# Kernel optimization log

Measured on AMD Instinct MI355X. Metric: run time of the kernel, lower is better.

Reference implementation:

```python
import jax, jax.numpy as jnp
import numpy as np

RFF_DIM = 256
ATTENTION_SCALE = 0.1
LAMBDA_REG = 0.01
SIGMA = 1.0


def setup_inputs() -> dict:
    key = jax.random.key(0)
    k1, k2, k3 = jax.random.split(key, 3)
    N, D_IN = 262144, 64
    Z = jax.random.normal(k1, (N, D_IN), dtype=jnp.float32)
    W_rff = jax.random.normal(k2, (D_IN, RFF_DIM), dtype=jnp.float32)
    A = jax.random.normal(k3, (2 * RFF_DIM, 3), dtype=jnp.float32) * 0.01
    return {"Z": Z, "W_rff": W_rff, "A": A}


def reference(Z, W_rff, A):
    # --- RFF transform: Q = sqrt(1/R) * [cos(Z W / sigma), sin(Z W / sigma)] ---
    proj = (Z @ W_rff) / SIGMA                       # [N, R]
    Q = jnp.sqrt(1.0 / RFF_DIM) * jnp.concatenate(
        [jnp.cos(proj), jnp.sin(proj)], axis=-1)      # [N, 2R]

    N, F = Q.shape
    chunk = max(F // RFF_DIM, 1)                      # = 2 here
    n_chunks = F // chunk                             # = RFF_DIM

    # --- convexified attention over feature chunks (vectorized) ---
    Qc = Q.reshape(N, n_chunks, chunk)                # [N, K, c]
    A_mean = jnp.mean(A, axis=-1)                     # [2R]
    # per-chunk trace score: mean over batch of <Q_i, A_mean[:c]>
    scores = jnp.mean(jnp.einsum('nkc,c->nk', Qc, A_mean[:chunk]), axis=0)  # [K]
    alpha = jax.nn.softmax(scores / (ATTENTION_SCALE * np.sqrt(RFF_DIM)))   # [K]
    # per-chunk reweighting (dim-preserving recombination)
    Q_tilde = (alpha[None, :, None] * Qc).reshape(N, F)                      # [N, 2R]

    # --- small GEMM head + nuclear-norm regularizer ---
    predictions = Q_tilde @ A                          # [N, out]
    AW = jax.nn.softmax(predictions / np.sqrt(RFF_DIM), axis=-1)
    nuclear_norm = jnp.sum(jnp.linalg.svd(A, compute_uv=False))
    reg_loss = LAMBDA_REG * nuclear_norm
    return predictions, AW, reg_loss, alpha
```

## Files before the change

### kernel.cpp

```cpp
#include <hip/hip_runtime.h>
#include <math.h>

#define N_ROWS 262144
#define D_IN 64
#define RFF 256
#define NTILES (N_ROWS / 16)
#define GRID_BIG 768
#define NWAVES (GRID_BIG * 4)

#define OFF_PRED 0
#define OFF_AW (N_ROWS * 3)
#define OFF_REG (2 * N_ROWS * 3)
#define OFF_ALPHA (2 * N_ROWS * 3 + 1)

#define WS_B 512
#define WS_WF 1280

typedef _Float16 f16x8 __attribute__((ext_vector_type(8)));
typedef float f32x4 __attribute__((ext_vector_type(4)));
typedef float f32x2 __attribute__((ext_vector_type(2)));

__device__ __forceinline__ f32x4 mfma16(f16x8 a, f16x8 b, f32x4 c) {
    return __builtin_amdgcn_mfma_f32_16x16x32_f16(a, b, c, 0, 0, 0);
}

__device__ __forceinline__ unsigned short f32_to_bf16_rne(float x) {
    unsigned int u = __float_as_uint(x);
    unsigned int r = u + 0x7fffu + ((u >> 16) & 1u);
    return (unsigned short)(r >> 16);
}

__device__ __forceinline__ void sincos_rev(float pr, float& sn, float& cs) {
    float f;
    asm("v_fract_f32 %0, %1" : "=v"(f) : "v"(pr));
    asm("v_sin_f32 %0, %1" : "=v"(sn) : "v"(f));
    asm("v_cos_f32 %0, %1" : "=v"(cs) : "v"(f));
}

__device__ __forceinline__ void gload_lds16(const float* g, float* lds) {
    __builtin_amdgcn_global_load_lds(
        (const __attribute__((address_space(1))) unsigned int*)g,
        (__attribute__((address_space(3))) unsigned int*)(lds), 16, 0, 0);
}

#define WAITVM0() do { asm volatile("s_waitcnt vmcnt(0)" ::: "memory"); \
                       __builtin_amdgcn_sched_barrier(0); } while (0)
#define LGKM0()   do { asm volatile("s_waitcnt lgkmcnt(0)" ::: "memory"); \
                       __builtin_amdgcn_sched_barrier(0); } while (0)

__global__ __launch_bounds__(256) void k_prep(const float* __restrict__ W,
                                              float* __restrict__ ws) {
    const int e = blockIdx.x * 256 + threadIdx.x;
    if (e < 512) ws[e] = 0.f;
    const int lane = e & 63;
    const int slot = e >> 6;
    const int kh = slot & 1;
    const int ct = slot >> 1;
    const int k0 = kh * 32 + 8 * (lane >> 4);
    const int col = ct * 16 + (lane & 15);
    f16x8 v;
#pragma unroll
    for (int i = 0; i < 8; ++i)
        v[i] = (_Float16)(W[(k0 + i) * RFF + col] * 0.15915494309189535f);
    *(f16x8*)(ws + WS_WF + e * 4) = v;
}

__device__ __forceinline__ void dma_Bf(const float* __restrict__ wsWf, float* Bff,
                                       int wv, int l) {
#pragma unroll
    for (int m = 0; m < 8; ++m) {
        const int off = wv * 2048 + m * 256;
        gload_lds16(wsWf + off + l * 4, Bff + off);
    }
}

__device__ __forceinline__ void stage_dma(const float* __restrict__ Z, int n0, int l,
                                          float* ldsbase) {
#pragma unroll
    for (int m = 0; m < 4; ++m) {
        const int row = m * 4 + (l >> 4);
        const int gc = (l & 15) ^ (row & 7);
        gload_lds16(Z + (size_t)(n0 + row) * D_IN + gc * 4, ldsbase + m * 256);
    }
}

__device__ __forceinline__ void frags_from_lds(const float* bb, int lr, int lh,
                                               f16x8& ah0, f16x8& ah1) {
    const int s4 = lr & 7;
    const float* rp = bb + lr * 64;
    float z[16];
    *(float4*)&z[0]  = *(const float4*)(rp + (((lh * 2 + 0) ^ s4) << 2));
    *(float4*)&z[4]  = *(const float4*)(rp + (((lh * 2 + 1) ^ s4) << 2));
    *(float4*)&z[8]  = *(const float4*)(rp + (((lh * 2 + 8) ^ s4) << 2));
    *(float4*)&z[12] = *(const float4*)(rp + (((lh * 2 + 9) ^ s4) << 2));
    LGKM0();
#pragma unroll
    for (int i = 0; i < 8; ++i) {
        ah0[i] = (_Float16)z[i];
        ah1[i] = (_Float16)z[8 + i];
    }
}

__global__ __launch_bounds__(256, 3) void k_pass1(const float* __restrict__ Z,
                                                  const float* __restrict__ ws_in,
                                                  float* __restrict__ U) {
    __shared__ float Bff[8192];
    __shared__ float Zs[4][1024];
    __shared__ float Ured[512];
    const int t = threadIdx.x;
    const int wv = t >> 6, l = t & 63, lr = l & 15, lh = l >> 4;

    dma_Bf(ws_in + WS_WF, Bff, wv, l);
    const int gwid = blockIdx.x * 4 + wv;
    const int tstart = gwid * 5 + (gwid < 1024 ? gwid : 1024);
    const int tcnt = 5 + (gwid < 1024 ? 1 : 0);
    stage_dma(Z, tstart * 16, l, &Zs[wv][0]);
    Ured[t] = 0.f;
    Ured[t + 256] = 0.f;
    __syncthreads();

    const f16x8* Bf = (const f16x8*)Bff;
    f32x2 accC2[16], accS2[16];
#pragma unroll
    for (int c = 0; c < 16; ++c) { accC2[c] = (f32x2){0.f, 0.f}; accS2[c] = (f32x2){0.f, 0.f}; }

    for (int tt = 0; tt < tcnt; ++tt) {
        if (tt) WAITVM0();
        f16x8 ah0, ah1;
        frags_from_lds(&Zs[wv][0], lr, lh, ah0, ah1);
        if (tt + 1 < tcnt) {
            stage_dma(Z, (tstart + tt + 1) * 16, l, &Zs[wv][0]);
            __builtin_amdgcn_sched_barrier(0);
        }
        f32x4 acc[16];
#pragma unroll
        for (int ct = 0; ct < 16; ++ct) acc[ct] = (f32x4){0.f, 0.f, 0.f, 0.f};
#pragma unroll
        for (int ct = 0; ct < 16; ++ct) {
            acc[ct] = mfma16(ah0, Bf[(ct * 2 + 0) * 64 + l], acc[ct]);
            acc[ct] = mfma16(ah1, Bf[(ct * 2 + 1) * 64 + l], acc[ct]);
        }
#pragma unroll
        for (int ct = 0; ct < 16; ++ct) {
            float sn0, cs0, sn1, cs1, sn2, cs2, sn3, cs3;
            sincos_rev(acc[ct][0], sn0, cs0);
            sincos_rev(acc[ct][1], sn1, cs1);
            sincos_rev(acc[ct][2], sn2, cs2);
            sincos_rev(acc[ct][3], sn3, cs3);
            accC2[ct] += (f32x2){cs0, cs1};
            accC2[ct] += (f32x2){cs2, cs3};
            accS2[ct] += (f32x2){sn0, sn1};
            accS2[ct] += (f32x2){sn2, sn3};
        }
    }
#pragma unroll
    for (int ct = 0; ct < 16; ++ct) {
        float c = accC2[ct][0] + accC2[ct][1];
        float s = accS2[ct][0] + accS2[ct][1];
        c += __shfl_xor(c, 16);
        c += __shfl_xor(c, 32);
        s += __shfl_xor(s, 16);
        s += __shfl_xor(s, 32);
        if (l < 16) {
            atomicAdd(&Ured[ct * 16 + l], c * 0.0625f);
            atomicAdd(&Ured[256 + ct * 16 + l], s * 0.0625f);
        }
    }
    __syncthreads();
    atomicAdd(&U[t], Ured[t]);
    atomicAdd(&U[t + 256], Ured[t + 256]);
}

__global__ __launch_bounds__(256) void k_alpha(const float* __restrict__ U,
                                               const float* __restrict__ A,
                                               float* __restrict__ ws,
                                               float* __restrict__ out) {
    __shared__ float sm[256];
    __shared__ double gred[256];
    __shared__ double G6[6];
    const int k = threadIdx.x;

    const float am0 = (A[0] + A[1] + A[2]) * (1.0f / 3.0f);
    const float am1 = (A[3] + A[4] + A[5]) * (1.0f / 3.0f);
    float score = (am0 * U[2 * k] + am1 * U[2 * k + 1]) * (1.0f / (float)N_ROWS);
    float x = score * (1.0f / 1.6f);

    sm[k] = x;
    __syncthreads();
    for (int s = 128; s > 0; s >>= 1) {
        if (k < s) sm[k] = fmaxf(sm[k], sm[k + s]);
        __syncthreads();
    }
    float mx = sm[0];
    __syncthreads();
    float e = __expf(x - mx);
    sm[k] = e;
    __syncthreads();
    for (int s = 128; s > 0; s >>= 1) {
        if (k < s) sm[k] += sm[k + s];
        __syncthreads();
    }
    float al = e / sm[0];
    out[OFF_ALPHA + k] = al;
    sm[k] = al;
    __syncthreads();

    {
        const float ac = 0.0625f * sm[k >> 1];
        const float as = 0.0625f * sm[128 + (k >> 1)];
        unsigned int* BtP = (unsigned int*)(ws + WS_B);
#pragma unroll
        for (int j = 0; j < 3; ++j) {
            float bc = ac * A[k * 3 + j];
            float bs = as * A[(256 + k) * 3 + j];
            unsigned int ulo = f32_to_bf16_rne(bc);
            unsigned int uhi = f32_to_bf16_rne(bs);
            BtP[k * 3 + j] = ulo | (uhi << 16);
        }
    }

    double af[2][3];
#pragma unroll
    for (int t2 = 0; t2 < 2; ++t2)
#pragma unroll
        for (int j = 0; j < 3; ++j) af[t2][j] = (double)A[(k + t2 * 256) * 3 + j];
    const int ei[6] = {0, 0, 0, 1, 1, 2};
    const int ej[6] = {0, 1, 2, 1, 2, 2};
    for (int eidx = 0; eidx < 6; ++eidx) {
        double p = af[0][ei[eidx]] * af[0][ej[eidx]] + af[1][ei[eidx]] * af[1][ej[eidx]];
        gred[k] = p;
        __syncthreads();
        for (int s = 128; s > 0; s >>= 1) {
            if (k < s) gred[k] += gred[k + s];
            __syncthreads();
        }
        if (k == 0) G6[eidx] = gred[0];
        __syncthreads();
    }
    if (k == 0) {
        double g00 = G6[0], g01 = G6[1], g02 = G6[2], g11 = G6[3], g12 = G6[4], g22 = G6[5];
        double q = (g00 + g11 + g22) / 3.0;
        double p1 = g01 * g01 + g02 * g02 + g12 * g12;
        double p2 = (g00 - q) * (g00 - q) + (g11 - q) * (g11 - q) + (g22 - q) * (g22 - q) + 2.0 * p1;
        double nuc;
        if (p2 < 1e-300) {
            nuc = 3.0 * sqrt(fmax(q, 0.0));
        } else {
            double p = sqrt(p2 / 6.0);
            double b00 = (g00 - q) / p, b11 = (g11 - q) / p, b22 = (g22 - q) / p;
            double b01 = g01 / p, b02 = g02 / p, b12 = g12 / p;
            double detB = b00 * (b11 * b22 - b12 * b12) - b01 * (b01 * b22 - b12 * b02) +
                          b02 * (b01 * b12 - b11 * b02);
            double rr = detB / 2.0;
            rr = fmin(1.0, fmax(-1.0, rr));
            double phi = acos(rr) / 3.0;
            double e1 = q + 2.0 * p * cos(phi);
            double e3 = q + 2.0 * p * cos(phi + 2.0943951023931953);
            double e2 = 3.0 * q - e1 - e3;
            nuc = sqrt(fmax(e1, 0.0)) + sqrt(fmax(e2, 0.0)) + sqrt(fmax(e3, 0.0));
        }
        out[OFF_REG] = (float)(0.01 * nuc);
    }
}

__global__ __launch_bounds__(256, 3) void k_pass2(const float* __restrict__ Z,
                                                  const float* __restrict__ ws_in,
                                                  float* __restrict__ out) {
    __shared__ float Bff[8192];
    __shared__ float Zs[4][1024];
    __shared__ unsigned int BtP[768];
    const int t = threadIdx.x;
    const int wv = t >> 6, l = t & 63, lr = l & 15, lh = l >> 4;

    dma_Bf(ws_in + WS_WF, Bff, wv, l);
    const int gwid = blockIdx.x * 4 + wv;
    const int tstart = gwid * 5 + (gwid < 1024 ? gwid : 1024);
    const int tcnt = 5 + (gwid < 1024 ? 1 : 0);
    stage_dma(Z, tstart * 16, l, &Zs[wv][0]);
    {
        const unsigned int* src = (const unsigned int*)(ws_in + WS_B);
        BtP[t] = src[t];
        BtP[t + 256] = src[t + 256];
        BtP[t + 512] = src[t + 512];
    }
    __syncthreads();

    const f16x8* Bf = (const f16x8*)Bff;

    for (int tt = 0; tt < tcnt; ++tt) {
        const int n0 = (tstart + tt) * 16;
        if (tt) WAITVM0();
        f16x8 ah0, ah1;
        frags_from_lds(&Zs[wv][0], lr, lh, ah0, ah1);
        if (tt + 1 < tcnt) {
            stage_dma(Z, (tstart + tt + 1) * 16, l, &Zs[wv][0]);
            __builtin_amdgcn_sched_barrier(0);
        }
        f32x4 acc[16];
#pragma unroll
        for (int ct = 0; ct < 16; ++ct) acc[ct] = (f32x4){0.f, 0.f, 0.f, 0.f};
#pragma unroll
        for (int ct = 0; ct < 16; ++ct) {
            acc[ct] = mfma16(ah0, Bf[(ct * 2 + 0) * 64 + l], acc[ct]);
            acc[ct] = mfma16(ah1, Bf[(ct * 2 + 1) * 64 + l], acc[ct]);
        }
        f32x2 pa01[3], pa23[3];
#pragma unroll
        for (int j = 0; j < 3; ++j) { pa01[j] = (f32x2){0.f, 0.f}; pa23[j] = (f32x2){0.f, 0.f}; }
#pragma unroll
        for (int ct = 0; ct < 16; ++ct) {
            const int f = ct * 16 + lr;
            unsigned int u0 = BtP[f * 3 + 0], u1 = BtP[f * 3 + 1], u2 = BtP[f * 3 + 2];
            float sn0, cs0, sn1, cs1, sn2, cs2, sn3, cs3;
            sincos_rev(acc[ct][0], sn0, cs0);
            sincos_rev(acc[ct][1], sn1, cs1);
            sincos_rev(acc[ct][2], sn2, cs2);
            sincos_rev(acc[ct][3], sn3, cs3);
            const f32x2 cs01 = {cs0, cs1}, cs23 = {cs2, cs3};
            const f32x2 sn01 = {sn0, sn1}, sn23 = {sn2, sn3};
            const float bcf[3] = {__uint_as_float(u0 << 16), __uint_as_float(u1 << 16),
                                  __uint_as_float(u2 << 16)};
            const float bsf[3] = {__uint_as_float(u0 & 0xffff0000u),
                                  __uint_as_float(u1 & 0xffff0000u),
                                  __uint_as_float(u2 & 0xffff0000u)};
#pragma unroll
            for (int j = 0; j < 3; ++j) {
                const f32x2 bc2 = {bcf[j], bcf[j]};
                const f32x2 bs2 = {bsf[j], bsf[j]};
                pa01[j] = __builtin_elementwise_fma(
                    cs01, bc2, __builtin_elementwise_fma(sn01, bs2, pa01[j]));
                pa23[j] = __builtin_elementwise_fma(
                    cs23, bc2, __builtin_elementwise_fma(sn23, bs2, pa23[j]));
            }
        }
        float pa[4][3];
#pragma unroll
        for (int j = 0; j < 3; ++j) {
            pa[0][j] = pa01[j][0];
            pa[1][j] = pa01[j][1];
            pa[2][j] = pa23[j][0];
            pa[3][j] = pa23[j][1];
        }
#pragma unroll
        for (int r = 0; r < 4; ++r)
#pragma unroll
            for (int j = 0; j < 3; ++j) {
                pa[r][j] += __shfl_xor(pa[r][j], 1);
                pa[r][j] += __shfl_xor(pa[r][j], 2);
                pa[r][j] += __shfl_xor(pa[r][j], 4);
                pa[r][j] += __shfl_xor(pa[r][j], 8);
            }
        float q0 = 0.f, q1 = 0.f, q2 = 0.f;
#pragma unroll
        for (int r = 0; r < 4; ++r)
            if (lr == r) { q0 = pa[r][0]; q1 = pa[r][1]; q2 = pa[r][2]; }
        if (lr < 4) {
            const size_t n = (size_t)n0 + 4 * lh + lr;
            out[OFF_PRED + n * 3 + 0] = q0;
            out[OFF_PRED + n * 3 + 1] = q1;
            out[OFF_PRED + n * 3 + 2] = q2;
            float x0 = q0 * 0.0625f, x1 = q1 * 0.0625f, x2 = q2 * 0.0625f;
            float m = fmaxf(x0, fmaxf(x1, x2));
            float e0 = __expf(x0 - m), e1 = __expf(x1 - m), e2 = __expf(x2 - m);
            float inv = 1.0f / (e0 + e1 + e2);
            out[OFF_AW + n * 3 + 0] = e0 * inv;
            out[OFF_AW + n * 3 + 1] = e1 * inv;
            out[OFF_AW + n * 3 + 2] = e2 * inv;
        }
    }
}

extern "C" void kernel_launch(void* const* d_in, const int* in_sizes, int n_in,
                              void* d_out, int out_size, void* d_ws, size_t ws_size,
                              hipStream_t stream) {
    const float* Z = (const float*)d_in[0];
    const float* W = (const float*)d_in[1];
    const float* A = (const float*)d_in[2];
    float* out = (float*)d_out;
    float* ws = (float*)d_ws;

    hipLaunchKernelGGL(k_prep, dim3(8), dim3(256), 0, stream, W, ws);
    hipLaunchKernelGGL(k_pass1, dim3(GRID_BIG), dim3(256), 0, stream, Z, ws, ws);
    hipLaunchKernelGGL(k_alpha, dim3(1), dim3(256), 0, stream, ws, A, ws, out);
    hipLaunchKernelGGL(k_pass2, dim3(GRID_BIG), dim3(256), 0, stream, Z, ws, out);
}
```

Baseline: 88.82 us.

## Split RFF features across block pairs, fold alpha into pass2, add softmax kernel

```diff
diff --git a/kernel.cpp b/kernel.cpp
--- a/kernel.cpp
+++ b/kernel.cpp
@@ -5,15 +5,13 @@
 #define D_IN 64
 #define RFF 256
 #define NTILES (N_ROWS / 16)
-#define GRID_BIG 768
-#define NWAVES (GRID_BIG * 4)
+#define GRID 1024
 
 #define OFF_PRED 0
 #define OFF_AW (N_ROWS * 3)
 #define OFF_REG (2 * N_ROWS * 3)
 #define OFF_ALPHA (2 * N_ROWS * 3 + 1)
 
-#define WS_B 512
 #define WS_WF 1280
 
 typedef _Float16 f16x8 __attribute__((ext_vector_type(8)));
@@ -65,12 +63,12 @@
     *(f16x8*)(ws + WS_WF + e * 4) = v;
 }
 
-__device__ __forceinline__ void dma_Bf(const float* __restrict__ wsWf, float* Bff,
-                                       int wv, int l) {
-#pragma unroll
-    for (int m = 0; m < 8; ++m) {
-        const int off = wv * 2048 + m * 256;
-        gload_lds16(wsWf + off + l * 4, Bff + off);
+__device__ __forceinline__ void dma_Bf_half(const float* __restrict__ wsWf, float* Bf,
+                                            int h, int wv, int l) {
+#pragma unroll
+    for (int m = 0; m < 4; ++m) {
+        const int off = wv * 1024 + m * 256;
+        gload_lds16(wsWf + h * 4096 + off + l * 4, Bf + off);
     }
 }
 
@@ -101,221 +99,212 @@
     }
 }
 
-__global__ __launch_bounds__(256, 3) void k_pass1(const float* __restrict__ Z,
+__global__ __launch_bounds__(256, 4) void k_pass1(const float* __restrict__ Z,
                                                   const float* __restrict__ ws_in,
                                                   float* __restrict__ U) {
-    __shared__ float Bff[8192];
+    __shared__ float Bff[4096];
     __shared__ float Zs[4][1024];
-    __shared__ float Ured[512];
+    __shared__ float Ured[256];
     const int t = threadIdx.x;
     const int wv = t >> 6, l = t & 63, lr = l & 15, lh = l >> 4;
-
-    dma_Bf(ws_in + WS_WF, Bff, wv, l);
-    const int gwid = blockIdx.x * 4 + wv;
-    const int tstart = gwid * 5 + (gwid < 1024 ? gwid : 1024);
-    const int tcnt = 5 + (gwid < 1024 ? 1 : 0);
+    const int h = blockIdx.x & 1;
+    const int g = blockIdx.x >> 1;
+
+    dma_Bf_half(ws_in + WS_WF, Bff, h, wv, l);
+    const int tstart = g * 32 + wv * 8;
     stage_dma(Z, tstart * 16, l, &Zs[wv][0]);
     Ured[t] = 0.f;
-    Ured[t + 256] = 0.f;
     __syncthreads();
 
     const f16x8* Bf = (const f16x8*)Bff;
-    f32x2 accC2[16], accS2[16];
-#pragma unroll
-    for (int c = 0; c < 16; ++c) { accC2[c] = (f32x2){0.f, 0.f}; accS2[c] = (f32x2){0.f, 0.f}; }
-
-    for (int tt = 0; tt < tcnt; ++tt) {
+    f32x2 accC2[8], accS2[8];
+#pragma unroll
+    for (int c = 0; c < 8; ++c) { accC2[c] = (f32x2){0.f, 0.f}; accS2[c] = (f32x2){0.f, 0.f}; }
+
+    for (int tt = 0; tt < 8; ++tt) {
         if (tt) WAITVM0();
         f16x8 ah0, ah1;
         frags_from_lds(&Zs[wv][0], lr, lh, ah0, ah1);
-        if (tt + 1 < tcnt) {
+        if (tt + 1 < 8) {
             stage_dma(Z, (tstart + tt + 1) * 16, l, &Zs[wv][0]);
             __builtin_amdgcn_sched_barrier(0);
         }
-        f32x4 acc[16];
-#pragma unroll
-        for (int ct = 0; ct < 16; ++ct) acc[ct] = (f32x4){0.f, 0.f, 0.f, 0.f};
-#pragma unroll
-        for (int ct = 0; ct < 16; ++ct) {
-            acc[ct] = mfma16(ah0, Bf[(ct * 2 + 0) * 64 + l], acc[ct]);
-            acc[ct] = mfma16(ah1, Bf[(ct * 2 + 1) * 64 + l], acc[ct]);
-        }
-#pragma unroll
-        for (int ct = 0; ct < 16; ++ct) {
+        f32x4 acc[8];
+#pragma unroll
+        for (int c = 0; c < 8; ++c) acc[c] = (f32x4){0.f, 0.f, 0.f, 0.f};
+#pragma unroll
+        for (int c = 0; c < 8; ++c) {
+            acc[c] = mfma16(ah0, Bf[(c * 2 + 0) * 64 + l], acc[c]);
+            acc[c] = mfma16(ah1, Bf[(c * 2 + 1) * 64 + l], acc[c]);
+        }
+#pragma unroll
+        for (int c = 0; c < 8; ++c) {
             float sn0, cs0, sn1, cs1, sn2, cs2, sn3, cs3;
-            sincos_rev(acc[ct][0], sn0, cs0);
-            sincos_rev(acc[ct][1], sn1, cs1);
-            sincos_rev(acc[ct][2], sn2, cs2);
-            sincos_rev(acc[ct][3], sn3, cs3);
-            accC2[ct] += (f32x2){cs0, cs1};
-            accC2[ct] += (f32x2){cs2, cs3};
-            accS2[ct] += (f32x2){sn0, sn1};
-            accS2[ct] += (f32x2){sn2, sn3};
-        }
-    }
-#pragma unroll
-    for (int ct = 0; ct < 16; ++ct) {
-        float c = accC2[ct][0] + accC2[ct][1];
-        float s = accS2[ct][0] + accS2[ct][1];
-        c += __shfl_xor(c, 16);
-        c += __shfl_xor(c, 32);
-        s += __shfl_xor(s, 16);
-        s += __shfl_xor(s, 32);
+            sincos_rev(acc[c][0], sn0, cs0);
+            sincos_rev(acc[c][1], sn1, cs1);
+            sincos_rev(acc[c][2], sn2, cs2);
+            sincos_rev(acc[c][3], sn3, cs3);
+            accC2[c] += (f32x2){cs0, cs1};
+            accC2[c] += (f32x2){cs2, cs3};
+            accS2[c] += (f32x2){sn0, sn1};
+            accS2[c] += (f32x2){sn2, sn3};
+        }
+    }
+#pragma unroll
+    for (int c = 0; c < 8; ++c) {
+        float cc = accC2[c][0] + accC2[c][1];
+        float ss = accS2[c][0] + accS2[c][1];
+        cc += __shfl_xor(cc, 16);
+        cc += __shfl_xor(cc, 32);
+        ss += __shfl_xor(ss, 16);
+        ss += __shfl_xor(ss, 32);
         if (l < 16) {
-            atomicAdd(&Ured[ct * 16 + l], c * 0.0625f);
-            atomicAdd(&Ured[256 + ct * 16 + l], s * 0.0625f);
-        }
-    }
-    __syncthreads();
-    atomicAdd(&U[t], Ured[t]);
-    atomicAdd(&U[t + 256], Ured[t + 256]);
-}
-
-__global__ __launch_bounds__(256) void k_alpha(const float* __restrict__ U,
-                                               const float* __restrict__ A,
-                                               float* __restrict__ ws,
-                                               float* __restrict__ out) {
-    __shared__ float sm[256];
-    __shared__ double gred[256];
+            atomicAdd(&Ured[c * 16 + l], cc * 0.0625f);
+            atomicAdd(&Ured[128 + c * 16 + l], ss * 0.0625f);
+        }
+    }
+    __syncthreads();
+    if (t < 128) atomicAdd(&U[128 * h + t], Ured[t]);
+    else atomicAdd(&U[256 + 128 * h + (t - 128)], Ured[t]);
+}
+
+__global__ __launch_bounds__(256, 4) void k_pass2(const float* __restrict__ Z,
+                                                  const float* __restrict__ ws_in,
+                                                  const float* __restrict__ A,
+                                                  float* __restrict__ out) {
+    __shared__ float Bff[4096];
+    __shared__ float Zs[4][1024];
+    __shared__ float sca[256];
+    __shared__ unsigned int BtP[384];
     __shared__ double G6[6];
-    const int k = threadIdx.x;
+    const int t = threadIdx.x;
+    const int wv = t >> 6, l = t & 63, lr = l & 15, lh = l >> 4;
+    const int h = blockIdx.x & 1;
+    const int g = blockIdx.x >> 1;
+
+    dma_Bf_half(ws_in + WS_WF, Bff, h, wv, l);
 
     const float am0 = (A[0] + A[1] + A[2]) * (1.0f / 3.0f);
     const float am1 = (A[3] + A[4] + A[5]) * (1.0f / 3.0f);
-    float score = (am0 * U[2 * k] + am1 * U[2 * k + 1]) * (1.0f / (float)N_ROWS);
-    float x = score * (1.0f / 1.6f);
-
-    sm[k] = x;
+    float x = (am0 * ws_in[2 * t] + am1 * ws_in[2 * t + 1]) *
+              (1.0f / (float)N_ROWS) * (1.0f / 1.6f);
+    sca[t] = x;
     __syncthreads();
     for (int s = 128; s > 0; s >>= 1) {
-        if (k < s) sm[k] = fmaxf(sm[k], sm[k + s]);
+        if (t < s) sca[t] = fmaxf(sca[t], sca[t + s]);
         __syncthreads();
     }
-    float mx = sm[0];
+    float mx = sca[0];
     __syncthreads();
     float e = __expf(x - mx);
-    sm[k] = e;
+    sca[t] = e;
     __syncthreads();
     for (int s = 128; s > 0; s >>= 1) {
-        if (k < s) sm[k] += sm[k + s];
+        if (t < s) sca[t] += sca[t + s];
         __syncthreads();
     }
-    float al = e / sm[0];
-    out[OFF_ALPHA + k] = al;
-    sm[k] = al;
-    __syncthreads();
-
-    {
-        const float ac = 0.0625f * sm[k >> 1];
-        const float as = 0.0625f * sm[128 + (k >> 1)];
-        unsigned int* BtP = (unsigned int*)(ws + WS_B);
+    float al = e / sca[0];
+    __syncthreads();
+    sca[t] = al;
+    __syncthreads();
+
+    if (blockIdx.x == 0) {
+        out[OFF_ALPHA + t] = al;
+        double* gred = (double*)&Zs[0][0];
+        double af[2][3];
+#pragma unroll
+        for (int t2 = 0; t2 < 2; ++t2)
+#pragma unroll
+            for (int j = 0; j < 3; ++j) af[t2][j] = (double)A[(t + t2 * 256) * 3 + j];
+        const int ei[6] = {0, 0, 0, 1, 1, 2};
+        const int ej[6] = {0, 1, 2, 1, 2, 2};
+        for (int eidx = 0; eidx < 6; ++eidx) {
+            double p = af[0][ei[eidx]] * af[0][ej[eidx]] + af[1][ei[eidx]] * af[1][ej[eidx]];
+            gred[t] = p;
+            __syncthreads();
+            for (int s = 128; s > 0; s >>= 1) {
+                if (t < s) gred[t] += gred[t + s];
+                __syncthreads();
+            }
+            if (t == 0) G6[eidx] = gred[0];
+            __syncthreads();
+        }
+        if (t == 0) {
+            double g00 = G6[0], g01 = G6[1], g02 = G6[2], g11 = G6[3], g12 = G6[4], g22 = G6[5];
+            double q = (g00 + g11 + g22) / 3.0;
+            double p1 = g01 * g01 + g02 * g02 + g12 * g12;
+            double p2 = (g00 - q) * (g00 - q) + (g11 - q) * (g11 - q) +
+                        (g22 - q) * (g22 - q) + 2.0 * p1;
+            double nuc;
+            if (p2 < 1e-300) {
+                nuc = 3.0 * sqrt(fmax(q, 0.0));
+            } else {
+                double p = sqrt(p2 / 6.0);
+                double b00 = (g00 - q) / p, b11 = (g11 - q) / p, b22 = (g22 - q) / p;
+                double b01 = g01 / p, b02 = g02 / p, b12 = g12 / p;
+                double detB = b00 * (b11 * b22 - b12 * b12) - b01 * (b01 * b22 - b12 * b02) +
+                              b02 * (b01 * b12 - b11 * b02);
+                double rr = fmin(1.0, fmax(-1.0, detB / 2.0));
+                double phi = acos(rr) / 3.0;
+                double e1 = q + 2.0 * p * cos(phi);
+                double e3 = q + 2.0 * p * cos(phi + 2.0943951023931953);
+                double e2 = 3.0 * q - e1 - e3;
+                nuc = sqrt(fmax(e1, 0.0)) + sqrt(fmax(e2, 0.0)) + sqrt(fmax(e3, 0.0));
+            }
+            out[OFF_REG] = (float)(0.01 * nuc);
+        }
+        __syncthreads();
+    }
+
+    if (t < 128) {
+        const int fg = 128 * h + t;
+        const float ac = 0.0625f * sca[fg >> 1];
+        const float as = 0.0625f * sca[128 + (fg >> 1)];
 #pragma unroll
         for (int j = 0; j < 3; ++j) {
-            float bc = ac * A[k * 3 + j];
-            float bs = as * A[(256 + k) * 3 + j];
+            float bc = ac * A[fg * 3 + j];
+            float bs = as * A[(256 + fg) * 3 + j];
             unsigned int ulo = f32_to_bf16_rne(bc);
             unsigned int uhi = f32_to_bf16_rne(bs);
-            BtP[k * 3 + j] = ulo | (uhi << 16);
-        }
-    }
-
-    double af[2][3];
-#pragma unroll
-    for (int t2 = 0; t2 < 2; ++t2)
-#pragma unroll
-        for (int j = 0; j < 3; ++j) af[t2][j] = (double)A[(k + t2 * 256) * 3 + j];
-    const int ei[6] = {0, 0, 0, 1, 1, 2};
-    const int ej[6] = {0, 1, 2, 1, 2, 2};
-    for (int eidx = 0; eidx < 6; ++eidx) {
-        double p = af[0][ei[eidx]] * af[0][ej[eidx]] + af[1][ei[eidx]] * af[1][ej[eidx]];
-        gred[k] = p;
-        __syncthreads();
-        for (int s = 128; s > 0; s >>= 1) {
-            if (k < s) gred[k] += gred[k + s];
-            __syncthreads();
-        }
-        if (k == 0) G6[eidx] = gred[0];
-        __syncthreads();
-    }
-    if (k == 0) {
-        double g00 = G6[0], g01 = G6[1], g02 = G6[2], g11 = G6[3], g12 = G6[4], g22 = G6[5];
-        double q = (g00 + g11 + g22) / 3.0;
-        double p1 = g01 * g01 + g02 * g02 + g12 * g12;
-        double p2 = (g00 - q) * (g00 - q) + (g11 - q) * (g11 - q) + (g22 - q) * (g22 - q) + 2.0 * p1;
-        double nuc;
-        if (p2 < 1e-300) {
-            nuc = 3.0 * sqrt(fmax(q, 0.0));
-        } else {
-            double p = sqrt(p2 / 6.0);
-            double b00 = (g00 - q) / p, b11 = (g11 - q) / p, b22 = (g22 - q) / p;
-            double b01 = g01 / p, b02 = g02 / p, b12 = g12 / p;
-            double detB = b00 * (b11 * b22 - b12 * b12) - b01 * (b01 * b22 - b12 * b02) +
-                          b02 * (b01 * b12 - b11 * b02);
-            double rr = detB / 2.0;
-            rr = fmin(1.0, fmax(-1.0, rr));
-            double phi = acos(rr) / 3.0;
-            double e1 = q + 2.0 * p * cos(phi);
-            double e3 = q + 2.0 * p * cos(phi + 2.0943951023931953);
-            double e2 = 3.0 * q - e1 - e3;
-            nuc = sqrt(fmax(e1, 0.0)) + sqrt(fmax(e2, 0.0)) + sqrt(fmax(e3, 0.0));
-        }
-        out[OFF_REG] = (float)(0.01 * nuc);
-    }
-}
-
-__global__ __launch_bounds__(256, 3) void k_pass2(const float* __restrict__ Z,
-                                                  const float* __restrict__ ws_in,
-                                                  float* __restrict__ out) {
-    __shared__ float Bff[8192];
-    __shared__ float Zs[4][1024];
-    __shared__ unsigned int BtP[768];
-    const int t = threadIdx.x;
-    const int wv = t >> 6, l = t & 63, lr = l & 15, lh = l >> 4;
-
-    dma_Bf(ws_in + WS_WF, Bff, wv, l);
-    const int gwid = blockIdx.x * 4 + wv;
-    const int tstart = gwid * 5 + (gwid < 1024 ? gwid : 1024);
-    const int tcnt = 5 + (gwid < 1024 ? 1 : 0);
+            BtP[t * 3 + j] = ulo | (uhi << 16);
+        }
+    }
+
+    const int tstart = g * 32 + wv * 8;
     stage_dma(Z, tstart * 16, l, &Zs[wv][0]);
-    {
-        const unsigned int* src = (const unsigned int*)(ws_in + WS_B);
-        BtP[t] = src[t];
-        BtP[t + 256] = src[t + 256];
-        BtP[t + 512] = src[t + 512];
-    }
     __syncthreads();
 
     const f16x8* Bf = (const f16x8*)Bff;
 
-    for (int tt = 0; tt < tcnt; ++tt) {
+    for (int tt = 0; tt < 8; ++tt) {
         const int n0 = (tstart + tt) * 16;
         if (tt) WAITVM0();
         f16x8 ah0, ah1;
         frags_from_lds(&Zs[wv][0], lr, lh, ah0, ah1);
-        if (tt + 1 < tcnt) {
+        if (tt + 1 < 8) {
             stage_dma(Z, (tstart + tt + 1) * 16, l, &Zs[wv][0]);
             __builtin_amdgcn_sched_barrier(0);
         }
-        f32x4 acc[16];
-#pragma unroll
-        for (int ct = 0; ct < 16; ++ct) acc[ct] = (f32x4){0.f, 0.f, 0.f, 0.f};
-#pragma unroll
-        for (int ct = 0; ct < 16; ++ct) {
-            acc[ct] = mfma16(ah0, Bf[(ct * 2 + 0) * 64 + l], acc[ct]);
-            acc[ct] = mfma16(ah1, Bf[(ct * 2 + 1) * 64 + l], acc[ct]);
+        f32x4 acc[8];
+#pragma unroll
+        for (int c = 0; c < 8; ++c) acc[c] = (f32x4){0.f, 0.f, 0.f, 0.f};
+#pragma unroll
+        for (int c = 0; c < 8; ++c) {
+            acc[c] = mfma16(ah0, Bf[(c * 2 + 0) * 64 + l], acc[c]);
+            acc[c] = mfma16(ah1, Bf[(c * 2 + 1) * 64 + l], acc[c]);
         }
         f32x2 pa01[3], pa23[3];
 #pragma unroll
         for (int j = 0; j < 3; ++j) { pa01[j] = (f32x2){0.f, 0.f}; pa23[j] = (f32x2){0.f, 0.f}; }
 #pragma unroll
-        for (int ct = 0; ct < 16; ++ct) {
-            const int f = ct * 16 + lr;
-            unsigned int u0 = BtP[f * 3 + 0], u1 = BtP[f * 3 + 1], u2 = BtP[f * 3 + 2];
+        for (int c = 0; c < 8; ++c) {
+            const int fl = c * 16 + lr;
+            unsigned int u0 = BtP[fl * 3 + 0], u1 = BtP[fl * 3 + 1], u2 = BtP[fl * 3 + 2];
             float sn0, cs0, sn1, cs1, sn2, cs2, sn3, cs3;
-            sincos_rev(acc[ct][0], sn0, cs0);
-            sincos_rev(acc[ct][1], sn1, cs1);
-            sincos_rev(acc[ct][2], sn2, cs2);
-            sincos_rev(acc[ct][3], sn3, cs3);
+            sincos_rev(acc[c][0], sn0, cs0);
+            sincos_rev(acc[c][1], sn1, cs1);
+            sincos_rev(acc[c][2], sn2, cs2);
+            sincos_rev(acc[c][3], sn3, cs3);
             const f32x2 cs01 = {cs0, cs1}, cs23 = {cs2, cs3};
             const f32x2 sn01 = {sn0, sn1}, sn23 = {sn2, sn3};
             const float bcf[3] = {__uint_as_float(u0 << 16), __uint_as_float(u1 << 16),
@@ -356,18 +345,25 @@
             if (lr == r) { q0 = pa[r][0]; q1 = pa[r][1]; q2 = pa[r][2]; }
         if (lr < 4) {
             const size_t n = (size_t)n0 + 4 * lh + lr;
-            out[OFF_PRED + n * 3 + 0] = q0;
-            out[OFF_PRED + n * 3 + 1] = q1;
-            out[OFF_PRED + n * 3 + 2] = q2;
-            float x0 = q0 * 0.0625f, x1 = q1 * 0.0625f, x2 = q2 * 0.0625f;
-            float m = fmaxf(x0, fmaxf(x1, x2));
-            float e0 = __expf(x0 - m), e1 = __expf(x1 - m), e2 = __expf(x2 - m);
-            float inv = 1.0f / (e0 + e1 + e2);
-            out[OFF_AW + n * 3 + 0] = e0 * inv;
-            out[OFF_AW + n * 3 + 1] = e1 * inv;
-            out[OFF_AW + n * 3 + 2] = e2 * inv;
-        }
-    }
+            atomicAdd(&out[OFF_PRED + n * 3 + 0], q0);
+            atomicAdd(&out[OFF_PRED + n * 3 + 1], q1);
+            atomicAdd(&out[OFF_PRED + n * 3 + 2], q2);
+        }
+    }
+}
+
+__global__ __launch_bounds__(256) void k_aw(float* __restrict__ out) {
+    const size_t n = (size_t)blockIdx.x * 256 + threadIdx.x;
+    const float p0 = out[OFF_PRED + n * 3 + 0];
+    const float p1 = out[OFF_PRED + n * 3 + 1];
+    const float p2 = out[OFF_PRED + n * 3 + 2];
+    const float x0 = p0 * 0.0625f, x1 = p1 * 0.0625f, x2 = p2 * 0.0625f;
+    const float m = fmaxf(x0, fmaxf(x1, x2));
+    const float e0 = __expf(x0 - m), e1 = __expf(x1 - m), e2 = __expf(x2 - m);
+    const float inv = 1.0f / (e0 + e1 + e2);
+    out[OFF_AW + n * 3 + 0] = e0 * inv;
+    out[OFF_AW + n * 3 + 1] = e1 * inv;
+    out[OFF_AW + n * 3 + 2] = e2 * inv;
 }
 
 extern "C" void kernel_launch(void* const* d_in, const int* in_sizes, int n_in,
@@ -379,8 +375,9 @@
     float* out = (float*)d_out;
     float* ws = (float*)d_ws;
 
+    (void)hipMemsetAsync(out, 0, (size_t)N_ROWS * 3 * sizeof(float), stream);
     hipLaunchKernelGGL(k_prep, dim3(8), dim3(256), 0, stream, W, ws);
-    hipLaunchKernelGGL(k_pass1, dim3(GRID_BIG), dim3(256), 0, stream, Z, ws, ws);
-    hipLaunchKernelGGL(k_alpha, dim3(1), dim3(256), 0, stream, ws, A, ws, out);
-    hipLaunchKernelGGL(k_pass2, dim3(GRID_BIG), dim3(256), 0, stream, Z, ws, out);
-}
+    hipLaunchKernelGGL(k_pass1, dim3(GRID), dim3(256), 0, stream, Z, ws, ws);
+    hipLaunchKernelGGL(k_pass2, dim3(GRID), dim3(256), 0, stream, Z, ws, A, out);
+    hipLaunchKernelGGL(k_aw, dim3(N_ROWS / 256), dim3(256), 0, stream, out);
+}
```

Result: no change. 88.33 us (-0.5%).
